# Performance work log

Measured on AMD Instinct MI355X. Metric: run time of the kernel, lower is better.

Reference implementation:

```python
import jax, jax.numpy as jnp
import numpy as np

NUM_OBJ_CLS = 151  # VG object classes incl. background
C = NUM_OBJ_CLS - 1  # multi-hot width = 150
PATH_DIM = 1024
B, P = 128, 512  # images, pairs per image


def setup_inputs() -> dict:
    key = jax.random.key(0)
    k1, k2, k3 = jax.random.split(key, 3)
    # predicted object-class labels per image; foreground classes 1..150
    pair_preds = jax.random.randint(k1, (B, P), 1, NUM_OBJ_CLS)
    W = jax.random.normal(k2, (PATH_DIM, C), dtype=jnp.float32) * 0.02
    b = jax.random.normal(k3, (PATH_DIM,), dtype=jnp.float32) * 0.02
    return {"pair_preds": pair_preds, "W": W, "b": b}


def reference(pair_preds, W, b):
    # Per image, build a multi-hot over the 150 foreground classes:
    # tmp[:, p-1] = 1 for every predicted label p (set is idempotent, so
    # the np.unique in the original is immaterial). Every row of an image
    # shares the same multi-hot vector.
    Bq, Pq = pair_preds.shape
    cols = pair_preds - 1  # [B, P]
    multi_hot = jnp.zeros((Bq, C), dtype=jnp.float32)
    multi_hot = multi_hot.at[jnp.arange(Bq)[:, None], cols].set(1.0)  # [B, C]
    # Each image contributes pairs.shape[0] = P identical rows, concatenated.
    context = jnp.repeat(multi_hot, Pq, axis=0)  # [B*P, C]
    # Linear projection: [B*P, C] @ [C, D] + [D]
    return context @ W.T + b
```

## Files before the change

kernel.cpp:

```cpp
#include <hip/hip_runtime.h>

#define NB   128
#define NP   512
#define NC   150
#define ND   1024
#define AD   64
#define ADB  (ND / AD)

typedef float  f4 __attribute__((ext_vector_type(4)));
typedef int    i4 __attribute__((ext_vector_type(4)));

__global__ __launch_bounds__(256) void labellayer_fused2(const int* __restrict__ preds,
                                                         const float* __restrict__ W,
                                                         const float* __restrict__ bias,
                                                         float* __restrict__ out) {
    __shared__ float wl[AD * NC];
    __shared__ float sflag[NC];
    __shared__ float part[4][AD];
    __shared__ float ys[AD];

    const unsigned bid  = blockIdx.x;
    const unsigned img  = bid >> 4;
    const unsigned dblk = bid & 15;
    const unsigned t    = threadIdx.x;

    i4 c4;
    if (t < NP / 4) c4 = ((const i4*)(preds + (size_t)img * NP))[t];

    if (t < NC) sflag[t] = 0.0f;

    const f4* wsrc = (const f4*)(W + (size_t)dblk * AD * NC);
    f4* wdst = (f4*)wl;
    #pragma unroll
    for (int i = 0; i < 10; ++i) {
        unsigned g = i * 256u + t;
        if (g < (AD * NC) / 4) wdst[g] = wsrc[g];
    }
    __syncthreads();

    if (t < NP / 4) {
        sflag[c4.x - 1] = 1.0f;
        sflag[c4.y - 1] = 1.0f;
        sflag[c4.z - 1] = 1.0f;
        sflag[c4.w - 1] = 1.0f;
    }
    __syncthreads();

    {
        const unsigned d  = t & 63;
        const unsigned q  = t >> 6;
        const unsigned c0 = q * 38;
        const unsigned c1 = (q == 3) ? NC : c0 + 38;
        float acc = 0.0f;
        const float* wrow = wl + (size_t)d * NC;
        for (unsigned c = c0; c < c1; ++c) {
            acc += sflag[c] * wrow[c];
        }
        part[q][d] = acc;
    }
    __syncthreads();

    if (t < AD) {
        ys[t] = bias[dblk * AD + t] + part[0][t] + part[1][t] + part[2][t] + part[3][t];
    }
    __syncthreads();

    const unsigned c  = t & 15;
    const unsigned r0 = t >> 4;
    const f4 v = ((const f4*)ys)[c];

    f4* o = (f4*)out + ((size_t)img << 17)
                     + ((size_t)dblk << 4) + c;
    #pragma unroll 8
    for (unsigned p = r0; p < NP; p += 16) {
        o[(size_t)p << 8] = v;
    }
}

extern "C" void kernel_launch(void* const* d_in, const int* in_sizes, int n_in,
                              void* d_out, int out_size, void* d_ws, size_t ws_size,
                              hipStream_t stream) {
    const int*   preds = (const int*)d_in[0];
    const float* W     = (const float*)d_in[1];
    const float* bias  = (const float*)d_in[2];
    float*       out   = (float*)d_out;

    labellayer_fused2<<<dim3(NB * ADB), dim3(256), 0, stream>>>(preds, W, bias, out);
}
```

Measured before the change: 49.78 us.

## Split block's output columns into two halves to overlap W load with stores

Each block now handles its 64 output columns as two halves of 32. The first half of W is staged into shared memory, and the second half is prefetched into registers while the first dot products run. The first half's output rows are written while the second half is computed. The aim is to hide the W load latency behind compute and the large output stores. In exchange the block takes more registers and extra barriers, and each store now writes 128-byte segments instead of 256-byte ones.

```diff
diff --git a/kernel.cpp b/kernel.cpp
--- a/kernel.cpp
+++ b/kernel.cpp
@@ -5,19 +5,20 @@
 #define NC   150
 #define ND   1024
 #define AD   64
+#define HD   32
 #define ADB  (ND / AD)
 
 typedef float  f4 __attribute__((ext_vector_type(4)));
 typedef int    i4 __attribute__((ext_vector_type(4)));
 
-__global__ __launch_bounds__(256) void labellayer_fused2(const int* __restrict__ preds,
-                                                         const float* __restrict__ W,
-                                                         const float* __restrict__ bias,
-                                                         float* __restrict__ out) {
+__global__ __launch_bounds__(256) void labellayer_pipe(const int* __restrict__ preds,
+                                                       const float* __restrict__ W,
+                                                       const float* __restrict__ bias,
+                                                       float* __restrict__ out) {
     __shared__ float wl[AD * NC];
     __shared__ float sflag[NC];
-    __shared__ float part[4][AD];
-    __shared__ float ys[AD];
+    __shared__ float part[8][HD];
+    __shared__ float ys[2][HD];
 
     const unsigned bid  = blockIdx.x;
     const unsigned img  = bid >> 4;
@@ -26,16 +27,20 @@
 
     i4 c4;
     if (t < NP / 4) c4 = ((const i4*)(preds + (size_t)img * NP))[t];
-
-    if (t < NC) sflag[t] = 0.0f;
+    float bv0 = 0.0f, bv1 = 0.0f;
+    if (t < HD) {
+        bv0 = bias[dblk * AD + t];
+        bv1 = bias[dblk * AD + HD + t];
+    }
 
     const f4* wsrc = (const f4*)(W + (size_t)dblk * AD * NC);
     f4* wdst = (f4*)wl;
     #pragma unroll
-    for (int i = 0; i < 10; ++i) {
+    for (int i = 0; i < 5; ++i) {
         unsigned g = i * 256u + t;
-        if (g < (AD * NC) / 4) wdst[g] = wsrc[g];
+        if (g < 1200u) wdst[g] = wsrc[g];
     }
+    if (t < NC) sflag[t] = 0.0f;
     __syncthreads();
 
     if (t < NP / 4) {
@@ -44,36 +49,70 @@
         sflag[c4.z - 1] = 1.0f;
         sflag[c4.w - 1] = 1.0f;
     }
+    f4 h1[5];
+    #pragma unroll
+    for (int i = 0; i < 5; ++i) {
+        unsigned g = 1200u + i * 256u + t;
+        if (g < 2400u) h1[i] = wsrc[g];
+    }
     __syncthreads();
 
+    const unsigned d  = t & 31;
+    const unsigned q  = t >> 5;
+    const unsigned c0 = q * 19;
+    const unsigned c1 = (c0 + 19 > NC) ? NC : c0 + 19;
     {
-        const unsigned d  = t & 63;
-        const unsigned q  = t >> 6;
-        const unsigned c0 = q * 38;
-        const unsigned c1 = (q == 3) ? NC : c0 + 38;
         float acc = 0.0f;
         const float* wrow = wl + (size_t)d * NC;
-        for (unsigned c = c0; c < c1; ++c) {
-            acc += sflag[c] * wrow[c];
-        }
+        for (unsigned c = c0; c < c1; ++c) acc += sflag[c] * wrow[c];
         part[q][d] = acc;
     }
     __syncthreads();
 
-    if (t < AD) {
-        ys[t] = bias[dblk * AD + t] + part[0][t] + part[1][t] + part[2][t] + part[3][t];
+    if (t < HD) {
+        ys[0][t] = bv0 + part[0][t] + part[1][t] + part[2][t] + part[3][t]
+                       + part[4][t] + part[5][t] + part[6][t] + part[7][t];
+    }
+    #pragma unroll
+    for (int i = 0; i < 5; ++i) {
+        unsigned g = 1200u + i * 256u + t;
+        if (g < 2400u) wdst[g] = h1[i];
     }
     __syncthreads();
 
-    const unsigned c  = t & 15;
-    const unsigned r0 = t >> 4;
-    const f4 v = ((const f4*)ys)[c];
+    const unsigned sc = t & 7;
+    const unsigned r0 = t >> 3;
+    {
+        const f4 v0 = ((const f4*)ys[0])[sc];
+        f4* o = (f4*)out + ((size_t)img << 17) + ((size_t)dblk << 4) + sc;
+        #pragma unroll 8
+        for (unsigned p = r0; p < NP; p += 32) {
+            o[(size_t)p << 8] = v0;
+        }
+    }
 
-    f4* o = (f4*)out + ((size_t)img << 17)
-                     + ((size_t)dblk << 4) + c;
-    #pragma unroll 8
-    for (unsigned p = r0; p < NP; p += 16) {
-        o[(size_t)p << 8] = v;
+    {
+        float acc = 0.0f;
+        const float* wrow = wl + 4800 + (size_t)d * NC;
+        for (unsigned c = c0; c < c1; ++c) acc += sflag[c] * wrow[c];
+        __syncthreads();
+        part[q][d] = acc;
+    }
+    __syncthreads();
+
+    if (t < HD) {
+        ys[1][t] = bv1 + part[0][t] + part[1][t] + part[2][t] + part[3][t]
+                       + part[4][t] + part[5][t] + part[6][t] + part[7][t];
+    }
+    __syncthreads();
+
+    {
+        const f4 v1 = ((const f4*)ys[1])[sc];
+        f4* o = (f4*)out + ((size_t)img << 17) + ((size_t)dblk << 4) + 8 + sc;
+        #pragma unroll 8
+        for (unsigned p = r0; p < NP; p += 32) {
+            o[(size_t)p << 8] = v1;
+        }
     }
 }
 
@@ -85,5 +124,5 @@
     const float* bias  = (const float*)d_in[2];
     float*       out   = (float*)d_out;
 
-    labellayer_fused2<<<dim3(NB * ADB), dim3(256), 0, stream>>>(preds, W, bias, out);
+    labellayer_pipe<<<dim3(NB * ADB), dim3(256), 0, stream>>>(preds, W, bias, out);
 }
```

Measured after the change: 49.56 us. Within noise of the previous version (-0.4%).
